# Kernel optimization log

Measured on AMD Instinct MI355X. Metric: run time of the kernel, lower is better.

## Reference

```python
import jax, jax.numpy as jnp
import numpy as np

N = 50000       # nodes
E = 800000      # edges (before self loops)
DIN = 128       # input feature width
H = 4           # heads
C = 64          # hidden width per head
NCLS = 2        # num classes
NEG_SLOPE = 0.2 # PyG GATConv default negative_slope


def setup_inputs() -> dict:
    key = jax.random.key(0)
    ks = jax.random.split(key, 16)
    x = jax.random.normal(ks[0], (N, DIN), dtype=jnp.float32)
    edge_index = jax.random.randint(ks[1], (2, E), 0, N, dtype=jnp.int64)
    s = 0.05
    # layer 0: DIN -> H*C
    W0 = jax.random.normal(ks[2], (DIN, H * C), dtype=jnp.float32) * s
    a_src0 = jax.random.normal(ks[3], (H, C), dtype=jnp.float32) * s
    a_dst0 = jax.random.normal(ks[4], (H, C), dtype=jnp.float32) * s
    b0 = jnp.zeros((H * C,), dtype=jnp.float32)
    # layer 1: H*C -> H*C
    W1 = jax.random.normal(ks[5], (H * C, H * C), dtype=jnp.float32) * s
    a_src1 = jax.random.normal(ks[6], (H, C), dtype=jnp.float32) * s
    a_dst1 = jax.random.normal(ks[7], (H, C), dtype=jnp.float32) * s
    b1 = jnp.zeros((H * C,), dtype=jnp.float32)
    # layer 2: H*C -> NCLS, single head
    W2 = jax.random.normal(ks[8], (H * C, NCLS), dtype=jnp.float32) * s
    a_src2 = jax.random.normal(ks[9], (1, NCLS), dtype=jnp.float32) * s
    a_dst2 = jax.random.normal(ks[10], (1, NCLS), dtype=jnp.float32) * s
    b2 = jnp.zeros((NCLS,), dtype=jnp.float32)
    return {"x": x, "edge_index": edge_index,
            "W0": W0, "a_src0": a_src0, "a_dst0": a_dst0, "b0": b0,
            "W1": W1, "a_src1": a_src1, "a_dst1": a_dst1, "b1": b1,
            "W2": W2, "a_src2": a_src2, "a_dst2": a_dst2, "b2": b2}


def gat_conv(x, ei, W, a_src, a_dst, b, heads, out_c):
    """PyG-style GATConv (add_self_loops already applied to ei, concat=True)."""
    n = x.shape[0]
    h = (x @ W).reshape(n, heads, out_c)              # [N, H, C]
    src, dst = ei[0], ei[1]
    asrc = (h * a_src).sum(-1)                         # [N, H]
    adst = (h * a_dst).sum(-1)                         # [N, H]
    alpha = jax.nn.leaky_relu(asrc[src] + adst[dst], NEG_SLOPE)  # [E', H]
    # segment softmax over incoming edges of each dst node
    amax = jax.ops.segment_max(alpha, dst, num_segments=n)        # [N, H]
    e = jnp.exp(alpha - amax[dst])
    denom = jax.ops.segment_sum(e, dst, num_segments=n)
    coef = e / denom[dst]                              # [E', H]
    msg = h[src] * coef[:, :, None]                    # [E', H, C]
    out = jax.ops.segment_sum(msg, dst, num_segments=n)           # [N, H, C]
    return out.reshape(n, heads * out_c) + b


def reference(x, edge_index, W0, a_src0, a_dst0, b0,
              W1, a_src1, a_dst1, b1, W2, a_src2, a_dst2, b2):
    # Inference mode: dropout(p=0.5, training=False) is identity.
    loops = jnp.arange(N, dtype=edge_index.dtype)
    ei = jnp.concatenate([edge_index, jnp.stack([loops, loops])], axis=1)
    h = jnp.tanh(gat_conv(x, ei, W0, a_src0, a_dst0, b0, H, C))
    h = jnp.tanh(gat_conv(h, ei, W1, a_src1, a_dst1, b1, H, C))
    h = gat_conv(h, ei, W2, a_src2, a_dst2, b2, 1, NCLS)
    return jax.nn.softmax(h, axis=1), h
```

## Files before the change

kernel.cpp:

```cpp
#include <hip/hip_runtime.h>
#include <hip/hip_bf16.h>

#define NEG 0.2f

typedef float f32x4 __attribute__((ext_vector_type(4)));
typedef short bf16x8 __attribute__((ext_vector_type(8)));

struct __align__(8) us4 { unsigned short v[4]; };

__device__ __forceinline__ float b2f(unsigned short u){
  union { unsigned int i; float f; } x; x.i = ((unsigned int)u) << 16; return x.f;
}
__device__ __forceinline__ unsigned short f2b(float f){
  __hip_bfloat16 h = __float2bfloat16(f);
  return *reinterpret_cast<unsigned short*>(&h);
}

__global__ __launch_bounds__(256) void k_setup(
    const float* __restrict__ W0, unsigned short* __restrict__ Wp0,
    const float* __restrict__ W1, unsigned short* __restrict__ Wp1,
    const int* __restrict__ ei, int* __restrict__ meta,
    int* __restrict__ deg, int N, int npack){
  const int bid = blockIdx.x;
  if (bid < npack){
    int t = bid*256 + threadIdx.x;
    const int T0 = 16*4*64;
    const int T1 = 16*8*64;
    const float* W; unsigned short* Wp;
    if (t < T0){ W = W0; Wp = Wp0; }
    else if (t < T0 + T1){ W = W1; Wp = Wp1; t -= T0; }
    else return;
    int lane = t & 63;
    int nb = (t >> 6) & 15;
    int kb = (t >> 6) >> 4;
    int kbase = kb*32 + ((lane>>4)<<3);
    int col = nb*16 + (lane&15);
    #pragma unroll
    for (int j=0;j<8;j++) Wp[(size_t)t*8 + j] = f2b(W[(size_t)(kbase+j)*256 + col]);
  } else {
    int i = (bid - npack)*256 + threadIdx.x;
    if (i < N) deg[i] = 0;
    if (i == 0){
      int o = 0;
      #pragma unroll
      for (int j=1;j<128;j+=2) o |= ei[j];
      meta[0] = (o==0) ? 1 : 0;
    }
  }
}

template<int K, int CVT>
__device__ __forceinline__ void gemm_body(int bid, const void* __restrict__ Xv,
    const unsigned short* __restrict__ Wp,
    const float* __restrict__ aS, const float* __restrict__ aD,
    unsigned short* __restrict__ Hout,
    float* __restrict__ asrc, float* __restrict__ adst, int N){
  constexpr int KB = K/32;
  __shared__ short sB[2][16*64*8];
  const int lane = threadIdx.x & 63;
  const int wave = threadIdx.x >> 6;
  const int rowbase = bid*64 + wave*16;
  const int l15 = lane & 15, lhi = lane >> 4;
  const int arow = rowbase + l15;

  bf16x8 aF[KB];
  if (CVT){
    const float* X = (const float*)Xv;
    #pragma unroll
    for (int kb=0; kb<KB; kb++){
      bf16x8 a = {};
      if (arow < N){
        f32x4 v0 = *(const f32x4*)(X + (size_t)arow*K + kb*32 + lhi*8);
        f32x4 v1 = *(const f32x4*)(X + (size_t)arow*K + kb*32 + lhi*8 + 4);
        #pragma unroll
        for (int j=0;j<4;j++){ a[j] = (short)f2b(v0[j]); a[j+4] = (short)f2b(v1[j]); }
      }
      aF[kb] = a;
    }
  } else {
    const unsigned short* X = (const unsigned short*)Xv;
    #pragma unroll
    for (int kb=0; kb<KB; kb++){
      bf16x8 a = {};
      if (arow < N) a = *(const bf16x8*)(X + (size_t)arow*K + kb*32 + lhi*8);
      aF[kb] = a;
    }
  }

  auto stage = [&](int buf, int kb){
    #pragma unroll
    for (int q=0;q<4;q++){
      int nb = wave*4 + q;
      const unsigned short* gsrc = Wp + ((size_t)((kb*16 + nb)*64) + lane)*8;
      __builtin_amdgcn_global_load_lds(
          (const __attribute__((address_space(1))) void*)gsrc,
          (__attribute__((address_space(3))) void*)&sB[buf][(size_t)nb*64*8],
          16, 0, 0);
    }
  };

  f32x4 acc[16] = {};
  stage(0, 0);
  __syncthreads();
  #pragma unroll
  for (int kb=0; kb<KB; kb++){
    const int cur = kb & 1;
    if (kb+1 < KB) stage(cur^1, kb+1);
    #pragma unroll
    for (int nb=0; nb<16; nb++){
      bf16x8 b = *(const bf16x8*)(&sB[cur][((size_t)nb*64 + lane)*8]);
      acc[nb] = __builtin_amdgcn_mfma_f32_16x16x32_bf16(aF[kb], b, acc[nb], 0, 0, 0);
    }
    __syncthreads();
  }

  const int r0 = rowbase + lhi*4;

  float sp[4][4] = {}; float dp[4][4] = {};
  #pragma unroll
  for (int h=0; h<4; h++){
    #pragma unroll
    for (int q=0; q<4; q++){
      const int nb = h*4 + q;
      float ws = aS[h*64 + q*16 + l15];
      float wd = aD[h*64 + q*16 + l15];
      #pragma unroll
      for (int r=0;r<4;r++){ sp[r][h] += acc[nb][r]*ws; dp[r][h] += acc[nb][r]*wd; }
    }
  }
  #pragma unroll
  for (int m=1;m<16;m<<=1){
    #pragma unroll
    for (int r=0;r<4;r++){
      #pragma unroll
      for (int h=0;h<4;h++){
        sp[r][h] += __shfl_xor(sp[r][h], m);
        dp[r][h] += __shfl_xor(dp[r][h], m);
      }
    }
  }
  if (l15 < 4){
    const int h = l15;
    #pragma unroll
    for (int r=0;r<4;r++){
      int row = r0 + r;
      if (row < N){ asrc[row*4+h] = sp[r][h]; adst[row*4+h] = dp[r][h]; }
    }
  }
  #pragma unroll
  for (int nb=0;nb<16;nb++){
    #pragma unroll
    for (int r=0;r<4;r++){
      int row = r0 + r;
      if (row < N) Hout[(size_t)row*256 + nb*16 + l15] = f2b(acc[nb][r]);
    }
  }
}

__global__ __launch_bounds__(256) void k_g128deg(
    const float* __restrict__ x, const unsigned short* __restrict__ Wp0,
    const float* __restrict__ aS, const float* __restrict__ aD,
    unsigned short* __restrict__ hb,
    float* __restrict__ asrc, float* __restrict__ adst, int N,
    const int* __restrict__ ei, const int* __restrict__ meta,
    int* __restrict__ deg, int E, int EP, int ngemm){
  const int bid = blockIdx.x;
  if (bid < ngemm){
    gemm_body<128,1>(bid, x, Wp0, aS, aD, hb, asrc, adst, N);
  } else {
    int base = ((bid - ngemm)*256 + threadIdx.x)*4;
    const int m0 = meta[0];
    #pragma unroll
    for (int j=0;j<4;j++){
      int e = base + j;
      if (e >= EP) break;
      int d;
      if (e < E) d = m0 ? ei[2*(size_t)(E+e)] : ei[E+e];
      else       d = e - E;
      if ((unsigned)d < (unsigned)N) atomicAdd(deg + d, 1);
    }
  }
}

__global__ __launch_bounds__(256) void k_gemm256(const unsigned short* __restrict__ X,
    const unsigned short* __restrict__ Wp,
    const float* __restrict__ aS, const float* __restrict__ aD,
    unsigned short* __restrict__ Hout,
    float* __restrict__ asrc, float* __restrict__ adst, int N){
  gemm_body<256,0>(blockIdx.x, X, Wp, aS, aD, Hout, asrc, adst, N);
}


__global__ void k_scan1(const int* __restrict__ deg, int* __restrict__ tmp,
                        int* __restrict__ bsum, int N){
  __shared__ int s[256];
  int t = threadIdx.x;
  int i = blockIdx.x*256 + t;
  int v = (i < N) ? deg[i] : 0;
  s[t] = v;
  __syncthreads();
  for (int off=1; off<256; off<<=1){
    int x = (t>=off) ? s[t-off] : 0;
    __syncthreads();
    s[t] += x;
    __syncthreads();
  }
  if (i < N) tmp[i] = s[t] - v;
  if (t == 255) bsum[blockIdx.x] = s[255];
}

__global__ void k_scan2(const int* __restrict__ bsum, int* __restrict__ bsumx,
                        int* __restrict__ meta, int n){
  __shared__ int s[256];
  int t = threadIdx.x;
  int v = (t < n) ? bsum[t] : 0;
  s[t] = v;
  __syncthreads();
  for (int off=1; off<256; off<<=1){
    int x = (t>=off) ? s[t-off] : 0;
    __syncthreads();
    s[t] += x;
    __syncthreads();
  }
  bsumx[t] = s[t] - v;
  if (t == 255) meta[1] = s[255];
}

__global__ void k_scan3(const int* __restrict__ tmp, const int* __restrict__ bsumx,
                        const int* __restrict__ meta,
                        int* __restrict__ rp, int* __restrict__ cur, int N){
  int i = blockIdx.x*256 + threadIdx.x;
  if (i < N){ int v = tmp[i] + bsumx[i>>8]; rp[i] = v; cur[i] = v; }
  if (i == 0) rp[N] = meta[1];
}

__global__ void k_fill(const int* __restrict__ ei, const int* __restrict__ meta,
                       int* __restrict__ cur, int* __restrict__ csr, int E, int EP, int N){
  int e = blockIdx.x*blockDim.x + threadIdx.x;
  if (e >= EP) return;
  int s, d;
  if (e < E){
    if (meta[0]){ s = ei[2*(size_t)e]; d = ei[2*(size_t)(E+e)]; }
    else        { s = ei[e];           d = ei[E+e]; }
  } else { s = d = e - E; }
  if ((unsigned)d >= (unsigned)N) return;
  int pos = atomicAdd(cur + d, 1);
  csr[pos] = s;
}

template<int FUSE2>
__global__ __launch_bounds__(256) void k_agg(const unsigned short* __restrict__ Hb,
    const float* __restrict__ asrc, const float* __restrict__ adst,
    const int* __restrict__ rp, const int* __restrict__ csr,
    const float* __restrict__ bias, unsigned short* __restrict__ Xout, int N,
    const float* __restrict__ W2, const float* __restrict__ as2,
    const float* __restrict__ ad2,
    float* __restrict__ H2, float* __restrict__ asrc2, float* __restrict__ adst2){
  const int lane = threadIdx.x & 63;
  const int dst = blockIdx.x*4 + (threadIdx.x >> 6);
  if (dst >= N) return;
  const int head = lane >> 4;
  const int c0 = lane*4;
  const float ad = adst[dst*4 + head];
  const int s0 = rp[dst], s1 = rp[dst+1];
  float a0=0.f,a1=0.f,a2=0.f,a3=0.f,den=0.f;
  int e = s0;
  for (; e+8 <= s1; e += 8){
    int i0 = csr[e+0], i1 = csr[e+1], i2 = csr[e+2], i3 = csr[e+3];
    int i4 = csr[e+4], i5 = csr[e+5], i6 = csr[e+6], i7 = csr[e+7];
    float x0 = asrc[(size_t)i0*4 + head];
    float x1 = asrc[(size_t)i1*4 + head];
    float x2 = asrc[(size_t)i2*4 + head];
    float x3 = asrc[(size_t)i3*4 + head];
    float x4 = asrc[(size_t)i4*4 + head];
    float x5 = asrc[(size_t)i5*4 + head];
    float x6 = asrc[(size_t)i6*4 + head];
    float x7 = asrc[(size_t)i7*4 + head];
    us4 h0 = *(const us4*)(Hb + (size_t)i0*256 + c0);
    us4 h1 = *(const us4*)(Hb + (size_t)i1*256 + c0);
    us4 h2 = *(const us4*)(Hb + (size_t)i2*256 + c0);
    us4 h3 = *(const us4*)(Hb + (size_t)i3*256 + c0);
    us4 h4 = *(const us4*)(Hb + (size_t)i4*256 + c0);
    us4 h5 = *(const us4*)(Hb + (size_t)i5*256 + c0);
    us4 h6 = *(const us4*)(Hb + (size_t)i6*256 + c0);
    us4 h7 = *(const us4*)(Hb + (size_t)i7*256 + c0);
    x0 += ad; x0 = x0 > 0.f ? x0 : NEG*x0; float e0 = __expf(x0);
    x1 += ad; x1 = x1 > 0.f ? x1 : NEG*x1; float e1 = __expf(x1);
    x2 += ad; x2 = x2 > 0.f ? x2 : NEG*x2; float e2 = __expf(x2);
    x3 += ad; x3 = x3 > 0.f ? x3 : NEG*x3; float e3 = __expf(x3);
    x4 += ad; x4 = x4 > 0.f ? x4 : NEG*x4; float e4 = __expf(x4);
    x5 += ad; x5 = x5 > 0.f ? x5 : NEG*x5; float e5 = __expf(x5);
    x6 += ad; x6 = x6 > 0.f ? x6 : NEG*x6; float e6 = __expf(x6);
    x7 += ad; x7 = x7 > 0.f ? x7 : NEG*x7; float e7 = __expf(x7);
    den += ((e0+e1)+(e2+e3)) + ((e4+e5)+(e6+e7));
    a0 += e0*b2f(h0.v[0]) + e1*b2f(h1.v[0]) + e2*b2f(h2.v[0]) + e3*b2f(h3.v[0])
        + e4*b2f(h4.v[0]) + e5*b2f(h5.v[0]) + e6*b2f(h6.v[0]) + e7*b2f(h7.v[0]);
    a1 += e0*b2f(h0.v[1]) + e1*b2f(h1.v[1]) + e2*b2f(h2.v[1]) + e3*b2f(h3.v[1])
        + e4*b2f(h4.v[1]) + e5*b2f(h5.v[1]) + e6*b2f(h6.v[1]) + e7*b2f(h7.v[1]);
    a2 += e0*b2f(h0.v[2]) + e1*b2f(h1.v[2]) + e2*b2f(h2.v[2]) + e3*b2f(h3.v[2])
        + e4*b2f(h4.v[2]) + e5*b2f(h5.v[2]) + e6*b2f(h6.v[2]) + e7*b2f(h7.v[2]);
    a3 += e0*b2f(h0.v[3]) + e1*b2f(h1.v[3]) + e2*b2f(h2.v[3]) + e3*b2f(h3.v[3])
        + e4*b2f(h4.v[3]) + e5*b2f(h5.v[3]) + e6*b2f(h6.v[3]) + e7*b2f(h7.v[3]);
  }
  for (; e+4 <= s1; e += 4){
    int i0 = csr[e+0], i1 = csr[e+1], i2 = csr[e+2], i3 = csr[e+3];
    float x0 = asrc[(size_t)i0*4 + head];
    float x1 = asrc[(size_t)i1*4 + head];
    float x2 = asrc[(size_t)i2*4 + head];
    float x3 = asrc[(size_t)i3*4 + head];
    us4 h0 = *(const us4*)(Hb + (size_t)i0*256 + c0);
    us4 h1 = *(const us4*)(Hb + (size_t)i1*256 + c0);
    us4 h2 = *(const us4*)(Hb + (size_t)i2*256 + c0);
    us4 h3 = *(const us4*)(Hb + (size_t)i3*256 + c0);
    x0 += ad; x0 = x0 > 0.f ? x0 : NEG*x0; float e0 = __expf(x0);
    x1 += ad; x1 = x1 > 0.f ? x1 : NEG*x1; float e1 = __expf(x1);
    x2 += ad; x2 = x2 > 0.f ? x2 : NEG*x2; float e2 = __expf(x2);
    x3 += ad; x3 = x3 > 0.f ? x3 : NEG*x3; float e3 = __expf(x3);
    den += (e0 + e1) + (e2 + e3);
    a0 += e0*b2f(h0.v[0]) + e1*b2f(h1.v[0]) + e2*b2f(h2.v[0]) + e3*b2f(h3.v[0]);
    a1 += e0*b2f(h0.v[1]) + e1*b2f(h1.v[1]) + e2*b2f(h2.v[1]) + e3*b2f(h3.v[1]);
    a2 += e0*b2f(h0.v[2]) + e1*b2f(h1.v[2]) + e2*b2f(h2.v[2]) + e3*b2f(h3.v[2]);
    a3 += e0*b2f(h0.v[3]) + e1*b2f(h1.v[3]) + e2*b2f(h2.v[3]) + e3*b2f(h3.v[3]);
  }
  for (; e < s1; e++){
    int src = csr[e];
    float al = asrc[(size_t)src*4 + head] + ad;
    al = al > 0.f ? al : NEG*al;
    float ee = __expf(al);
    den += ee;
    us4 hv = *(const us4*)(Hb + (size_t)src*256 + c0);
    a0 += ee * b2f(hv.v[0]);
    a1 += ee * b2f(hv.v[1]);
    a2 += ee * b2f(hv.v[2]);
    a3 += ee * b2f(hv.v[3]);
  }
  float rd = 1.0f/den;
  f32x4 bv = *(const f32x4*)(bias + c0);
  float o0 = tanhf(a0*rd + bv[0]);
  float o1 = tanhf(a1*rd + bv[1]);
  float o2 = tanhf(a2*rd + bv[2]);
  float o3 = tanhf(a3*rd + bv[3]);
  if (FUSE2){
    f32x4 w01 = *(const f32x4*)(W2 + c0*2);
    f32x4 w23 = *(const f32x4*)(W2 + c0*2 + 4);
    float p0 = o0*w01[0] + o1*w01[2] + o2*w23[0] + o3*w23[2];
    float p1 = o0*w01[1] + o1*w01[3] + o2*w23[1] + o3*w23[3];
    #pragma unroll
    for (int m=1;m<64;m<<=1){ p0 += __shfl_xor(p0,m); p1 += __shfl_xor(p1,m); }
    if (lane == 0){
      H2[(size_t)dst*2+0] = p0;
      H2[(size_t)dst*2+1] = p1;
      asrc2[dst] = p0*as2[0] + p1*as2[1];
      adst2[dst] = p0*ad2[0] + p1*ad2[1];
    }
  } else {
    us4 o;
    o.v[0] = f2b(o0); o.v[1] = f2b(o1); o.v[2] = f2b(o2); o.v[3] = f2b(o3);
    *(us4*)(Xout + (size_t)dst*256 + c0) = o;
  }
}

__global__ __launch_bounds__(256) void k_agg2(const float* __restrict__ H2,
    const float* __restrict__ asrc2, const float* __restrict__ adst2,
    const int* __restrict__ rp, const int* __restrict__ csr, const float* __restrict__ bb,
    float* __restrict__ out, int N){
  const int sub = threadIdx.x & 15;
  const int dst = blockIdx.x*16 + (threadIdx.x >> 4);
  if (dst >= N) return;
  const float ad = adst2[dst];
  const int s0 = rp[dst], s1 = rp[dst+1];
  float n0=0.f, n1=0.f, den=0.f;
  for (int e=s0+sub; e<s1; e+=16){
    int src = csr[e];
    float al = asrc2[src] + ad;
    al = al>0.f ? al : NEG*al;
    float ee = __expf(al);
    den += ee;
    n0 += ee * H2[src*2+0];
    n1 += ee * H2[src*2+1];
  }
  #pragma unroll
  for (int m=1;m<16;m<<=1){
    n0 += __shfl_xor(n0,m); n1 += __shfl_xor(n1,m); den += __shfl_xor(den,m);
  }
  if (sub==0){
    float o0 = n0/den + bb[0];
    float o1 = n1/den + bb[1];
    float mx = fmaxf(o0,o1);
    float e0 = __expf(o0-mx), e1 = __expf(o1-mx);
    float is = 1.0f/(e0+e1);
    out[(size_t)dst*2+0] = e0*is;
    out[(size_t)dst*2+1] = e1*is;
    out[(size_t)2*N + dst*2+0] = o0;
    out[(size_t)2*N + dst*2+1] = o1;
  }
}

extern "C" void kernel_launch(void* const* d_in, const int* in_sizes, int n_in,
                              void* d_out, int out_size, void* d_ws, size_t ws_size,
                              hipStream_t stream){
  const float* x  = (const float*)d_in[0];
  const int*   ei = (const int*)d_in[1];
  const float* W0 = (const float*)d_in[2];
  const float* as0= (const float*)d_in[3];
  const float* ad0= (const float*)d_in[4];
  const float* b0 = (const float*)d_in[5];
  const float* W1 = (const float*)d_in[6];
  const float* as1= (const float*)d_in[7];
  const float* ad1= (const float*)d_in[8];
  const float* b1 = (const float*)d_in[9];
  const float* W2 = (const float*)d_in[10];
  const float* as2= (const float*)d_in[11];
  const float* ad2= (const float*)d_in[12];
  const float* b2 = (const float*)d_in[13];

  const int N  = in_sizes[0] / 128;
  const int E  = in_sizes[1] / 2;
  const int EP = E + N;
  float* outp = (float*)d_out;

  char* w = (char*)d_ws;
  size_t off = 0;
  auto alloc = [&](size_t bytes)->char*{
    char* p = w + off; off = (off + bytes + 255) & ~(size_t)255; return p;
  };
  unsigned short* hb  = (unsigned short*)alloc((size_t)N*256*2);
  unsigned short* xa  = (unsigned short*)alloc((size_t)N*256*2);
  float* asrc  = (float*)alloc((size_t)N*4*4);
  float* adst  = (float*)alloc((size_t)N*4*4);
  float* asrc2 = (float*)alloc((size_t)N*4);
  float* adst2 = (float*)alloc((size_t)N*4);
  float* H2    = (float*)alloc((size_t)N*2*4);
  unsigned short* Wp0 = (unsigned short*)alloc((size_t)128*256*2);
  unsigned short* Wp1 = (unsigned short*)alloc((size_t)256*256*2);
  int* deg   = (int*)alloc((size_t)N*4);
  int* rp    = (int*)alloc((size_t)(N+1)*4);
  int* cur   = (int*)alloc((size_t)N*4);
  int* tmp   = (int*)alloc((size_t)N*4);
  int* bsum  = (int*)alloc(256*4);
  int* bsumx = (int*)alloc(256*4);
  int* meta  = (int*)alloc(8*4);
  int* csr   = (int*)alloc((size_t)EP*4);
  (void)ws_size; (void)n_in; (void)out_size;

  const int npack = (16*4*64 + 16*8*64) / 256;
  const int ninit = (N + 255)/256;
  k_setup<<<npack + ninit, 256, 0, stream>>>(W0, Wp0, W1, Wp1, ei, meta, deg, N, npack);

  const int ngemm = (N + 63)/64;
  const int ndeg  = (EP + 1023)/1024;
  k_g128deg<<<ngemm + ndeg, 256, 0, stream>>>(x, Wp0, as0, ad0, hb, asrc, adst, N,
                                              ei, meta, deg, E, EP, ngemm);

  const int nb1 = (N + 255)/256;
  k_scan1 <<<nb1, 256, 0, stream>>>(deg, tmp, bsum, N);
  k_scan2 <<<1, 256, 0, stream>>>(bsum, bsumx, meta, nb1);
  k_scan3 <<<nb1, 256, 0, stream>>>(tmp, bsumx, meta, rp, cur, N);
  k_fill  <<<(EP + 255)/256, 256, 0, stream>>>(ei, meta, cur, csr, E, EP, N);

  k_agg<0><<<(N + 3)/4, 256, 0, stream>>>(hb, asrc, adst, rp, csr, b0, xa, N,
                                          nullptr, nullptr, nullptr, nullptr, nullptr, nullptr);
  k_gemm256<<<ngemm, 256, 0, stream>>>(xa, Wp1, as1, ad1, hb, asrc, adst, N);
  k_agg<1><<<(N + 3)/4, 256, 0, stream>>>(hb, asrc, adst, rp, csr, b1, nullptr, N,
                                          W2, as2, ad2, H2, asrc2, adst2);
  k_agg2  <<<(N + 15)/16, 256, 0, stream>>>(H2, asrc2, adst2, rp, csr, b2, outp, N);
}
```

Baseline: 278.1 us.

## Split wavefront into two edge halves with 16-byte feature gathers in k_agg

The aggregation kernel now has each lane load 8 bf16 channels with one 16-byte gather instead of 4 channels with an 8-byte gather. The two 32-lane halves of the wavefront each process 4 of every 8 edges and combine partial sums with a cross-half shuffle. The scalar remainder loops are replaced by a single predicated tail. This is meant to cut the number of gather instructions and raise memory-level parallelism per wave. In exchange it adds reduction shuffles, and the tail does redundant clamped loads.

New measurement: 382.1 us. 37.4% more time.

```diff
diff --git a/kernel.cpp b/kernel.cpp
--- a/kernel.cpp
+++ b/kernel.cpp
@@ -4,9 +4,12 @@
 #define NEG 0.2f
 
 typedef float f32x4 __attribute__((ext_vector_type(4)));
+typedef float f32x2 __attribute__((ext_vector_type(2)));
 typedef short bf16x8 __attribute__((ext_vector_type(8)));
+typedef unsigned int u32x4 __attribute__((ext_vector_type(4)));
 
 struct __align__(8) us4 { unsigned short v[4]; };
+struct __align__(16) us8 { unsigned short v[8]; };
 
 __device__ __forceinline__ float b2f(unsigned short u){
   union { unsigned int i; float f; } x; x.i = ((unsigned int)u) << 16; return x.f;
@@ -14,6 +17,12 @@
 __device__ __forceinline__ unsigned short f2b(float f){
   __hip_bfloat16 h = __float2bfloat16(f);
   return *reinterpret_cast<unsigned short*>(&h);
+}
+__device__ __forceinline__ f32x2 bpair(unsigned int w){
+  union { unsigned int i; float f; } lo, hi;
+  lo.i = w << 16;
+  hi.i = w & 0xFFFF0000u;
+  f32x2 r; r[0] = lo.f; r[1] = hi.f; return r;
 }
 
 __global__ __launch_bounds__(256) void k_setup(
@@ -259,94 +268,85 @@
   const int lane = threadIdx.x & 63;
   const int dst = blockIdx.x*4 + (threadIdx.x >> 6);
   if (dst >= N) return;
-  const int head = lane >> 4;
-  const int c0 = lane*4;
+  const int half = lane >> 5;
+  const int l32 = lane & 31;
+  const int head = l32 >> 3;
+  const int c0 = l32*8;
   const float ad = adst[dst*4 + head];
   const int s0 = rp[dst], s1 = rp[dst+1];
-  float a0=0.f,a1=0.f,a2=0.f,a3=0.f,den=0.f;
+  f32x2 acc[4] = {};
+  float den = 0.f;
   int e = s0;
   for (; e+8 <= s1; e += 8){
-    int i0 = csr[e+0], i1 = csr[e+1], i2 = csr[e+2], i3 = csr[e+3];
-    int i4 = csr[e+4], i5 = csr[e+5], i6 = csr[e+6], i7 = csr[e+7];
+    const int base = e + (half<<2);
+    int i0 = csr[base+0], i1 = csr[base+1], i2 = csr[base+2], i3 = csr[base+3];
     float x0 = asrc[(size_t)i0*4 + head];
     float x1 = asrc[(size_t)i1*4 + head];
     float x2 = asrc[(size_t)i2*4 + head];
     float x3 = asrc[(size_t)i3*4 + head];
-    float x4 = asrc[(size_t)i4*4 + head];
-    float x5 = asrc[(size_t)i5*4 + head];
-    float x6 = asrc[(size_t)i6*4 + head];
-    float x7 = asrc[(size_t)i7*4 + head];
-    us4 h0 = *(const us4*)(Hb + (size_t)i0*256 + c0);
-    us4 h1 = *(const us4*)(Hb + (size_t)i1*256 + c0);
-    us4 h2 = *(const us4*)(Hb + (size_t)i2*256 + c0);
-    us4 h3 = *(const us4*)(Hb + (size_t)i3*256 + c0);
-    us4 h4 = *(const us4*)(Hb + (size_t)i4*256 + c0);
-    us4 h5 = *(const us4*)(Hb + (size_t)i5*256 + c0);
-    us4 h6 = *(const us4*)(Hb + (size_t)i6*256 + c0);
-    us4 h7 = *(const us4*)(Hb + (size_t)i7*256 + c0);
-    x0 += ad; x0 = x0 > 0.f ? x0 : NEG*x0; float e0 = __expf(x0);
-    x1 += ad; x1 = x1 > 0.f ? x1 : NEG*x1; float e1 = __expf(x1);
-    x2 += ad; x2 = x2 > 0.f ? x2 : NEG*x2; float e2 = __expf(x2);
-    x3 += ad; x3 = x3 > 0.f ? x3 : NEG*x3; float e3 = __expf(x3);
-    x4 += ad; x4 = x4 > 0.f ? x4 : NEG*x4; float e4 = __expf(x4);
-    x5 += ad; x5 = x5 > 0.f ? x5 : NEG*x5; float e5 = __expf(x5);
-    x6 += ad; x6 = x6 > 0.f ? x6 : NEG*x6; float e6 = __expf(x6);
-    x7 += ad; x7 = x7 > 0.f ? x7 : NEG*x7; float e7 = __expf(x7);
-    den += ((e0+e1)+(e2+e3)) + ((e4+e5)+(e6+e7));
-    a0 += e0*b2f(h0.v[0]) + e1*b2f(h1.v[0]) + e2*b2f(h2.v[0]) + e3*b2f(h3.v[0])
-        + e4*b2f(h4.v[0]) + e5*b2f(h5.v[0]) + e6*b2f(h6.v[0]) + e7*b2f(h7.v[0]);
-    a1 += e0*b2f(h0.v[1]) + e1*b2f(h1.v[1]) + e2*b2f(h2.v[1]) + e3*b2f(h3.v[1])
-        + e4*b2f(h4.v[1]) + e5*b2f(h5.v[1]) + e6*b2f(h6.v[1]) + e7*b2f(h7.v[1]);
-    a2 += e0*b2f(h0.v[2]) + e1*b2f(h1.v[2]) + e2*b2f(h2.v[2]) + e3*b2f(h3.v[2])
-        + e4*b2f(h4.v[2]) + e5*b2f(h5.v[2]) + e6*b2f(h6.v[2]) + e7*b2f(h7.v[2]);
-    a3 += e0*b2f(h0.v[3]) + e1*b2f(h1.v[3]) + e2*b2f(h2.v[3]) + e3*b2f(h3.v[3])
-        + e4*b2f(h4.v[3]) + e5*b2f(h5.v[3]) + e6*b2f(h6.v[3]) + e7*b2f(h7.v[3]);
-  }
-  for (; e+4 <= s1; e += 4){
-    int i0 = csr[e+0], i1 = csr[e+1], i2 = csr[e+2], i3 = csr[e+3];
-    float x0 = asrc[(size_t)i0*4 + head];
-    float x1 = asrc[(size_t)i1*4 + head];
-    float x2 = asrc[(size_t)i2*4 + head];
-    float x3 = asrc[(size_t)i3*4 + head];
-    us4 h0 = *(const us4*)(Hb + (size_t)i0*256 + c0);
-    us4 h1 = *(const us4*)(Hb + (size_t)i1*256 + c0);
-    us4 h2 = *(const us4*)(Hb + (size_t)i2*256 + c0);
-    us4 h3 = *(const us4*)(Hb + (size_t)i3*256 + c0);
+    u32x4 h0 = *(const u32x4*)(Hb + (size_t)i0*256 + c0);
+    u32x4 h1 = *(const u32x4*)(Hb + (size_t)i1*256 + c0);
+    u32x4 h2 = *(const u32x4*)(Hb + (size_t)i2*256 + c0);
+    u32x4 h3 = *(const u32x4*)(Hb + (size_t)i3*256 + c0);
     x0 += ad; x0 = x0 > 0.f ? x0 : NEG*x0; float e0 = __expf(x0);
     x1 += ad; x1 = x1 > 0.f ? x1 : NEG*x1; float e1 = __expf(x1);
     x2 += ad; x2 = x2 > 0.f ? x2 : NEG*x2; float e2 = __expf(x2);
     x3 += ad; x3 = x3 > 0.f ? x3 : NEG*x3; float e3 = __expf(x3);
     den += (e0 + e1) + (e2 + e3);
-    a0 += e0*b2f(h0.v[0]) + e1*b2f(h1.v[0]) + e2*b2f(h2.v[0]) + e3*b2f(h3.v[0]);
-    a1 += e0*b2f(h0.v[1]) + e1*b2f(h1.v[1]) + e2*b2f(h2.v[1]) + e3*b2f(h3.v[1]);
-    a2 += e0*b2f(h0.v[2]) + e1*b2f(h1.v[2]) + e2*b2f(h2.v[2]) + e3*b2f(h3.v[2]);
-    a3 += e0*b2f(h0.v[3]) + e1*b2f(h1.v[3]) + e2*b2f(h2.v[3]) + e3*b2f(h3.v[3]);
-  }
-  for (; e < s1; e++){
-    int src = csr[e];
-    float al = asrc[(size_t)src*4 + head] + ad;
-    al = al > 0.f ? al : NEG*al;
-    float ee = __expf(al);
-    den += ee;
-    us4 hv = *(const us4*)(Hb + (size_t)src*256 + c0);
-    a0 += ee * b2f(hv.v[0]);
-    a1 += ee * b2f(hv.v[1]);
-    a2 += ee * b2f(hv.v[2]);
-    a3 += ee * b2f(hv.v[3]);
-  }
-  float rd = 1.0f/den;
-  f32x4 bv = *(const f32x4*)(bias + c0);
-  float o0 = tanhf(a0*rd + bv[0]);
-  float o1 = tanhf(a1*rd + bv[1]);
-  float o2 = tanhf(a2*rd + bv[2]);
-  float o3 = tanhf(a3*rd + bv[3]);
+    #pragma unroll
+    for (int j=0;j<4;j++){
+      acc[j] += e0*bpair(h0[j]);
+      acc[j] += e1*bpair(h1[j]);
+      acc[j] += e2*bpair(h2[j]);
+      acc[j] += e3*bpair(h3[j]);
+    }
+  }
+  if (e < s1){
+    const int base = e + (half<<2);
+    #pragma unroll
+    for (int j=0;j<4;j++){
+      int idx = base + j;
+      bool v = idx < s1;
+      int src = csr[v ? idx : s1-1];
+      float x = asrc[(size_t)src*4 + head] + ad;
+      x = x > 0.f ? x : NEG*x;
+      float ee = v ? __expf(x) : 0.f;
+      den += ee;
+      u32x4 hv = *(const u32x4*)(Hb + (size_t)src*256 + c0);
+      acc[0] += ee*bpair(hv[0]);
+      acc[1] += ee*bpair(hv[1]);
+      acc[2] += ee*bpair(hv[2]);
+      acc[3] += ee*bpair(hv[3]);
+    }
+  }
+  den += __shfl_xor(den, 32);
+  #pragma unroll
+  for (int j=0;j<4;j++){
+    acc[j][0] += __shfl_xor(acc[j][0], 32);
+    acc[j][1] += __shfl_xor(acc[j][1], 32);
+  }
+  const float rd = 1.0f/den;
+  f32x4 bv0 = *(const f32x4*)(bias + c0);
+  f32x4 bv1 = *(const f32x4*)(bias + c0 + 4);
+  float o0 = tanhf(acc[0][0]*rd + bv0[0]);
+  float o1 = tanhf(acc[0][1]*rd + bv0[1]);
+  float o2 = tanhf(acc[1][0]*rd + bv0[2]);
+  float o3 = tanhf(acc[1][1]*rd + bv0[3]);
+  float o4 = tanhf(acc[2][0]*rd + bv1[0]);
+  float o5 = tanhf(acc[2][1]*rd + bv1[1]);
+  float o6 = tanhf(acc[3][0]*rd + bv1[2]);
+  float o7 = tanhf(acc[3][1]*rd + bv1[3]);
   if (FUSE2){
-    f32x4 w01 = *(const f32x4*)(W2 + c0*2);
-    f32x4 w23 = *(const f32x4*)(W2 + c0*2 + 4);
-    float p0 = o0*w01[0] + o1*w01[2] + o2*w23[0] + o3*w23[2];
-    float p1 = o0*w01[1] + o1*w01[3] + o2*w23[1] + o3*w23[3];
-    #pragma unroll
-    for (int m=1;m<64;m<<=1){ p0 += __shfl_xor(p0,m); p1 += __shfl_xor(p1,m); }
+    f32x4 wA = *(const f32x4*)(W2 + c0*2);
+    f32x4 wB = *(const f32x4*)(W2 + c0*2 + 4);
+    f32x4 wC = *(const f32x4*)(W2 + c0*2 + 8);
+    f32x4 wD = *(const f32x4*)(W2 + c0*2 + 12);
+    float p0 = o0*wA[0] + o1*wA[2] + o2*wB[0] + o3*wB[2]
+             + o4*wC[0] + o5*wC[2] + o6*wD[0] + o7*wD[2];
+    float p1 = o0*wA[1] + o1*wA[3] + o2*wB[1] + o3*wB[3]
+             + o4*wC[1] + o5*wC[3] + o6*wD[1] + o7*wD[3];
+    #pragma unroll
+    for (int m=1;m<32;m<<=1){ p0 += __shfl_xor(p0,m); p1 += __shfl_xor(p1,m); }
     if (lane == 0){
       H2[(size_t)dst*2+0] = p0;
       H2[(size_t)dst*2+1] = p1;
@@ -354,9 +354,12 @@
       adst2[dst] = p0*ad2[0] + p1*ad2[1];
     }
   } else {
-    us4 o;
-    o.v[0] = f2b(o0); o.v[1] = f2b(o1); o.v[2] = f2b(o2); o.v[3] = f2b(o3);
-    *(us4*)(Xout + (size_t)dst*256 + c0) = o;
+    if (lane < 32){
+      us8 o;
+      o.v[0] = f2b(o0); o.v[1] = f2b(o1); o.v[2] = f2b(o2); o.v[3] = f2b(o3);
+      o.v[4] = f2b(o4); o.v[5] = f2b(o5); o.v[6] = f2b(o6); o.v[7] = f2b(o7);
+      *(us8*)(Xout + (size_t)dst*256 + c0) = o;
+    }
   }
 }
 
```

## Replace three-kernel prefix scan with single-pass decoupled look-back scan

Applied to the files above, without the earlier changes.

Merges the three scan kernels (block scan, block-sum scan, add-back) into one kernel that uses a decoupled look-back over per-block status words held in a packed 64-bit array. The pack array is zeroed in the setup kernel. This removes two kernel launches and the temp-array round trip. In exchange it relies on earlier blocks making forward progress while later blocks spin-wait, and it adds serial look-back latency.

Measured after the change: 318.1 us. 1.14x slower.

```diff
diff --git a/kernel.cpp b/kernel.cpp
--- a/kernel.cpp
+++ b/kernel.cpp
@@ -20,7 +20,8 @@
     const float* __restrict__ W0, unsigned short* __restrict__ Wp0,
     const float* __restrict__ W1, unsigned short* __restrict__ Wp1,
     const int* __restrict__ ei, int* __restrict__ meta,
-    int* __restrict__ deg, int N, int npack){
+    int* __restrict__ deg, unsigned long long* __restrict__ pack,
+    int N, int npack, int nscan){
   const int bid = blockIdx.x;
   if (bid < npack){
     int t = bid*256 + threadIdx.x;
@@ -40,6 +41,7 @@
   } else {
     int i = (bid - npack)*256 + threadIdx.x;
     if (i < N) deg[i] = 0;
+    if (i < nscan) pack[i] = 0ull;
     if (i == 0){
       int o = 0;
       #pragma unroll
@@ -190,13 +192,14 @@
   gemm_body<256,0>(blockIdx.x, X, Wp, aS, aD, Hout, asrc, adst, N);
 }
 
-
-__global__ void k_scan1(const int* __restrict__ deg, int* __restrict__ tmp,
-                        int* __restrict__ bsum, int N){
+__global__ __launch_bounds__(256) void k_scanall(const int* __restrict__ deg,
+    int* __restrict__ rp, int* __restrict__ cur,
+    unsigned long long* __restrict__ pack, int N, int nb){
   __shared__ int s[256];
-  int t = threadIdx.x;
-  int i = blockIdx.x*256 + t;
-  int v = (i < N) ? deg[i] : 0;
+  __shared__ int sprefix;
+  const int bid = blockIdx.x, t = threadIdx.x;
+  const int i = bid*256 + t;
+  const int v = (i < N) ? deg[i] : 0;
   s[t] = v;
   __syncthreads();
   for (int off=1; off<256; off<<=1){
@@ -205,33 +208,29 @@
     s[t] += x;
     __syncthreads();
   }
-  if (i < N) tmp[i] = s[t] - v;
-  if (t == 255) bsum[blockIdx.x] = s[255];
-}
-
-__global__ void k_scan2(const int* __restrict__ bsum, int* __restrict__ bsumx,
-                        int* __restrict__ meta, int n){
-  __shared__ int s[256];
-  int t = threadIdx.x;
-  int v = (t < n) ? bsum[t] : 0;
-  s[t] = v;
+  const int total = s[255];
+  if (t == 0){
+    __hip_atomic_store(&pack[bid], (1ull<<32) | (unsigned)total,
+                       __ATOMIC_RELEASE, __HIP_MEMORY_SCOPE_AGENT);
+    long long run = 0;
+    int j = bid - 1;
+    while (j >= 0){
+      unsigned long long p;
+      do {
+        p = __hip_atomic_load(&pack[j], __ATOMIC_ACQUIRE, __HIP_MEMORY_SCOPE_AGENT);
+      } while ((p >> 32) == 0);
+      run += (int)(p & 0xffffffffu);
+      if ((p >> 32) == 2) break;
+      j--;
+    }
+    __hip_atomic_store(&pack[bid], (2ull<<32) | (unsigned)(run + total),
+                       __ATOMIC_RELEASE, __HIP_MEMORY_SCOPE_AGENT);
+    sprefix = (int)run;
+  }
   __syncthreads();
-  for (int off=1; off<256; off<<=1){
-    int x = (t>=off) ? s[t-off] : 0;
-    __syncthreads();
-    s[t] += x;
-    __syncthreads();
-  }
-  bsumx[t] = s[t] - v;
-  if (t == 255) meta[1] = s[255];
-}
-
-__global__ void k_scan3(const int* __restrict__ tmp, const int* __restrict__ bsumx,
-                        const int* __restrict__ meta,
-                        int* __restrict__ rp, int* __restrict__ cur, int N){
-  int i = blockIdx.x*256 + threadIdx.x;
-  if (i < N){ int v = tmp[i] + bsumx[i>>8]; rp[i] = v; cur[i] = v; }
-  if (i == 0) rp[N] = meta[1];
+  const int ex = sprefix + s[t] - v;
+  if (i < N){ rp[i] = ex; cur[i] = ex; }
+  if (bid == nb-1 && t == 255) rp[N] = sprefix + total;
 }
 
 __global__ void k_fill(const int* __restrict__ ei, const int* __restrict__ meta,
@@ -436,27 +435,24 @@
   int* deg   = (int*)alloc((size_t)N*4);
   int* rp    = (int*)alloc((size_t)(N+1)*4);
   int* cur   = (int*)alloc((size_t)N*4);
-  int* tmp   = (int*)alloc((size_t)N*4);
-  int* bsum  = (int*)alloc(256*4);
-  int* bsumx = (int*)alloc(256*4);
+  unsigned long long* pack = (unsigned long long*)alloc(512*8);
   int* meta  = (int*)alloc(8*4);
   int* csr   = (int*)alloc((size_t)EP*4);
   (void)ws_size; (void)n_in; (void)out_size;
 
   const int npack = (16*4*64 + 16*8*64) / 256;
   const int ninit = (N + 255)/256;
-  k_setup<<<npack + ninit, 256, 0, stream>>>(W0, Wp0, W1, Wp1, ei, meta, deg, N, npack);
+  const int nb1 = (N + 255)/256;
+  k_setup<<<npack + ninit, 256, 0, stream>>>(W0, Wp0, W1, Wp1, ei, meta, deg, pack,
+                                             N, npack, nb1);
 
   const int ngemm = (N + 63)/64;
   const int ndeg  = (EP + 1023)/1024;
   k_g128deg<<<ngemm + ndeg, 256, 0, stream>>>(x, Wp0, as0, ad0, hb, asrc, adst, N,
                                               ei, meta, deg, E, EP, ngemm);
 
-  const int nb1 = (N + 255)/256;
-  k_scan1 <<<nb1, 256, 0, stream>>>(deg, tmp, bsum, N);
-  k_scan2 <<<1, 256, 0, stream>>>(bsum, bsumx, meta, nb1);
-  k_scan3 <<<nb1, 256, 0, stream>>>(tmp, bsumx, meta, rp, cur, N);
-  k_fill  <<<(EP + 255)/256, 256, 0, stream>>>(ei, meta, cur, csr, E, EP, N);
+  k_scanall<<<nb1, 256, 0, stream>>>(deg, rp, cur, pack, N, nb1);
+  k_fill   <<<(EP + 255)/256, 256, 0, stream>>>(ei, meta, cur, csr, E, EP, N);
 
   k_agg<0><<<(N + 3)/4, 256, 0, stream>>>(hb, asrc, adst, rp, csr, b0, xa, N,
                                           nullptr, nullptr, nullptr, nullptr, nullptr, nullptr);
```
